# Performance work log

Hardware: AMD Instinct MI355X
Metric: run time of the kernel (lower is better)

The kernel has to match this reference:

```python
import jax, jax.numpy as jnp
import numpy as np

DIM = 384
NUM_HEADS = 12
HEAD_DIM = DIM // NUM_HEADS  # 32
SCALE = HEAD_DIM ** -0.5
B, N = 4, 2048


def setup_inputs() -> dict:
    key = jax.random.key(0)
    k0, k1, k2, k3 = jax.random.split(key, 4)
    x = jax.random.normal(k0, (B, N, DIM), dtype=jnp.float32)
    # nn.Linear(dim, 3*dim, bias=False): y = x @ W_qkv, W_qkv is [C, 3C]
    W_qkv = jax.random.normal(k1, (DIM, 3 * DIM), dtype=jnp.float32) * (DIM ** -0.5)
    # nn.Linear(dim, dim): y = x @ W_proj + b_proj, W_proj is [C, C]
    W_proj = jax.random.normal(k2, (DIM, DIM), dtype=jnp.float32) * (DIM ** -0.5)
    b_proj = jax.random.normal(k3, (DIM,), dtype=jnp.float32) * 0.01
    return {"x": x, "W_qkv": W_qkv, "W_proj": W_proj, "b_proj": b_proj}


def reference(x, W_qkv, W_proj, b_proj):
    b, n, c = x.shape
    qkv = (x @ W_qkv).reshape(b, n, 3, NUM_HEADS, HEAD_DIM)
    qkv = jnp.transpose(qkv, (2, 0, 3, 1, 4))  # [3, B, H, N, hd]
    q, k, v = qkv[0], qkv[1], qkv[2]
    # full attention: softmax(q k^T * scale) v
    attn = jnp.einsum('bhqd,bhkd->bhqk', q, k) * SCALE  # [B,H,N,N]
    attn = jax.nn.softmax(attn, axis=-1)
    out = jnp.einsum('bhqk,bhkd->bhqd', attn, v)  # [B,H,N,hd]
    out = jnp.transpose(out, (0, 2, 1, 3)).reshape(b, n, c)
    return out @ W_proj + b_proj
```

## Files before the change

kernel.cpp:

```cpp
#include <hip/hip_runtime.h>

constexpr int BB  = 4;
constexpr int SEQ = 2048;
constexpr int CC  = 384;
constexpr int C3  = 1152;
constexpr int NH  = 12;
constexpr int HD  = 32;
constexpr float SCALE = 0.17677669529663689f;
constexpr float LOG2E = 1.4426950408889634f;
constexpr float KSC   = SCALE * LOG2E;
constexpr size_t KV_BYTES = (size_t)2 * BB * NH * SEQ * HD * 2;
constexpr size_t WT_BYTES = ((size_t)C3 * CC + (size_t)CC * CC) * 2;
constexpr size_t XB_BYTES = (size_t)BB * SEQ * CC * 2;

typedef __attribute__((ext_vector_type(8))) short short8_t;
typedef __attribute__((ext_vector_type(4))) float floatx4;

#if __has_builtin(__builtin_amdgcn_exp2f)
#define EXP2F __builtin_amdgcn_exp2f
#else
#define EXP2F __builtin_exp2f
#endif

__device__ __forceinline__ unsigned short f2bf(float f) {
    unsigned int u = __builtin_bit_cast(unsigned int, f);
    u += 0x7fffu + ((u >> 16) & 1u);
    return (unsigned short)(u >> 16);
}
__device__ __forceinline__ unsigned int pk_rn(float lo, float hi) {
    return __builtin_amdgcn_perm(__builtin_bit_cast(unsigned int, hi) + 0x8000u,
                                 __builtin_bit_cast(unsigned int, lo) + 0x8000u,
                                 0x07060302u);
}
__device__ __forceinline__ unsigned int cvtpk(float lo, float hi) {
    unsigned int r;
    asm("v_cvt_pk_bf16_f32 %0, %1, %2" : "=v"(r) : "v"(lo), "v"(hi));
    return r;
}
__device__ __forceinline__ short8_t pack8(float4 a, float4 b) {
    uint4 u;
    u.x = pk_rn(a.x, a.y); u.y = pk_rn(a.z, a.w);
    u.z = pk_rn(b.x, b.y); u.w = pk_rn(b.z, b.w);
    return __builtin_bit_cast(short8_t, u);
}

__device__ __forceinline__ void vstore(unsigned short* vb, short8_t a, short8_t b) {
    const uint4 ua = __builtin_bit_cast(uint4, a);
    const uint4 ub = __builtin_bit_cast(uint4, b);
    *(uint2*)(vb)      = (uint2){ua.x, ua.y};
    *(uint2*)(vb + 8)  = (uint2){ua.z, ua.w};
    *(uint2*)(vb + 16) = (uint2){ub.x, ub.y};
    *(uint2*)(vb + 24) = (uint2){ub.z, ub.w};
}

__global__ __launch_bounds__(256) void prep_kernel(
    const float* __restrict__ x, const float* __restrict__ wqkv,
    const float* __restrict__ wproj,
    unsigned short* __restrict__ wqkvT, unsigned short* __restrict__ wprojT,
    unsigned short* __restrict__ xb)
{
    const int bid = blockIdx.x;
    if (bid >= 144) {
        const size_t base = (size_t)(bid - 144) * 2048 + threadIdx.x * 8;
        const float4 a = *(const float4*)(x + base);
        const float4 b = *(const float4*)(x + base + 4);
        uint4 u;
        u.x = pk_rn(a.x, a.y); u.y = pk_rn(a.z, a.w);
        u.z = pk_rn(b.x, b.y); u.w = pk_rn(b.z, b.w);
        *(uint4*)(xb + base) = u;
        return;
    }
    __shared__ float ls[64][68];
    const float* src; unsigned short* dst; int SN, k0, n0;
    if (bid < 108) {
        src = wqkv; dst = wqkvT; SN = C3;
        k0 = (bid / 18) * 64; n0 = (bid % 18) * 64;
    } else {
        const int b2 = bid - 108;
        src = wproj; dst = wprojT; SN = CC;
        k0 = (b2 / 6) * 64; n0 = (b2 % 6) * 64;
    }
    const int t  = threadIdx.x;
    const int rr = t >> 4, cc4 = (t & 15) * 4;
#pragma unroll
    for (int p = 0; p < 4; ++p) {
        const int row = p * 16 + rr;
        const float4 v = *(const float4*)&src[(size_t)(k0 + row) * SN + n0 + cc4];
        ls[row][cc4] = v.x; ls[row][cc4 + 1] = v.y;
        ls[row][cc4 + 2] = v.z; ls[row][cc4 + 3] = v.w;
    }
    __syncthreads();
#pragma unroll
    for (int p = 0; p < 4; ++p) {
        const int nrow = p * 16 + rr;
        uint2 u;
        u.x = pk_rn(ls[cc4][nrow],     ls[cc4 + 1][nrow]);
        u.y = pk_rn(ls[cc4 + 2][nrow], ls[cc4 + 3][nrow]);
        *(uint2*)&dst[(size_t)(n0 + nrow) * CC + k0 + cc4] = u;
    }
}

__global__ __launch_bounds__(256) void qkv_fast(
    const unsigned short* __restrict__ xb,
    const unsigned short* __restrict__ wT,
    unsigned short* __restrict__ qb,
    unsigned short* __restrict__ kv)
{
    __shared__ __align__(16) unsigned short As[2][128][40];
    __shared__ __align__(16) unsigned short Bs[2][128][40];

    const int mt   = blockIdx.x & 63;
    const int nb   = blockIdx.x >> 6;
    const int tid  = threadIdx.x;
    const int wid  = tid >> 6;
    const int lane = tid & 63;
    const int quad = lane >> 4;
    const int col  = lane & 15;
    const int wr   = wid >> 1, wc = wid & 1;
    const int m0 = mt * 128, n0 = nb * 128;

    const int arow = tid >> 1;
    const int aoff = (tid & 1) * 16;

    floatx4 acc[4][4];
#pragma unroll
    for (int i = 0; i < 4; ++i)
#pragma unroll
        for (int j = 0; j < 4; ++j) acc[i][j] = (floatx4){0.f, 0.f, 0.f, 0.f};

    const unsigned short* xrow = xb + (size_t)(m0 + arow) * CC + aoff;
    const unsigned short* wrow = wT + (size_t)(n0 + arow) * CC + aoff;

    short8_t ast0, ast1, bst0, bst1;
    ast0 = *(const short8_t*)xrow;
    ast1 = *(const short8_t*)(xrow + 8);
    bst0 = *(const short8_t*)wrow;
    bst1 = *(const short8_t*)(wrow + 8);
    *(short8_t*)&As[0][arow][aoff]     = ast0;
    *(short8_t*)&As[0][arow][aoff + 8] = ast1;
    *(short8_t*)&Bs[0][arow][aoff]     = bst0;
    *(short8_t*)&Bs[0][arow][aoff + 8] = bst1;

    for (int it = 0; it < CC / 32; ++it) {
        const int kn = (it + 1 < CC / 32) ? (it + 1) * 32 : 0;
        ast0 = *(const short8_t*)(xrow + kn);
        ast1 = *(const short8_t*)(xrow + kn + 8);
        bst0 = *(const short8_t*)(wrow + kn);
        bst1 = *(const short8_t*)(wrow + kn + 8);

        __syncthreads();
        const int p = it & 1;
        short8_t af[4], bf[4];
#pragma unroll
        for (int i = 0; i < 4; ++i)
            af[i] = *(const short8_t*)&As[p][wr * 64 + i * 16 + col][quad * 8];
#pragma unroll
        for (int j = 0; j < 4; ++j)
            bf[j] = *(const short8_t*)&Bs[p][wc * 64 + j * 16 + col][quad * 8];
#pragma unroll
        for (int j = 0; j < 4; ++j)
#pragma unroll
            for (int i = 0; i < 4; ++i)
                acc[i][j] = __builtin_amdgcn_mfma_f32_16x16x32_bf16(af[i], bf[j], acc[i][j], 0, 0, 0);

        *(short8_t*)&As[p ^ 1][arow][aoff]     = ast0;
        *(short8_t*)&As[p ^ 1][arow][aoff + 8] = ast1;
        *(short8_t*)&Bs[p ^ 1][arow][aoff]     = bst0;
        *(short8_t*)&Bs[p ^ 1][arow][aoff + 8] = bst1;
    }

    const int t = nb / 3;
#pragma unroll
    for (int i = 0; i < 4; ++i) {
        const int mg = m0 + wr * 64 + i * 16 + quad * 4;
        if (t == 0) {
#pragma unroll
            for (int j = 0; j < 4; ++j) {
                const int n = n0 + wc * 64 + j * 16 + col;
#pragma unroll
                for (int r = 0; r < 4; ++r)
                    qb[(size_t)(mg + r) * CC + n] = f2bf(acc[i][j][r]);
            }
        } else if (t == 1) {
            const int b = mg >> 11, s = mg & (SEQ - 1);
#pragma unroll
            for (int j = 0; j < 4; ++j) {
                const int rem = n0 - CC + wc * 64 + j * 16 + col;
                const int h = rem >> 5, d = rem & 31;
                unsigned short* kp = kv + ((size_t)(b * NH + h) * SEQ + s) * HD + d;
#pragma unroll
                for (int r = 0; r < 4; ++r)
                    kp[(size_t)r * HD] = f2bf(acc[i][j][r] * KSC);
            }
        } else {
            const int b = mg >> 11, s = mg & (SEQ - 1);
            unsigned short* vtb = kv + (size_t)BB * NH * SEQ * HD;
#pragma unroll
            for (int j = 0; j < 4; ++j) {
                const int rem = n0 - 2 * CC + wc * 64 + j * 16 + col;
                const int h = rem >> 5, d = rem & 31;
                uint2 u;
                u.x = pk_rn(acc[i][j][0], acc[i][j][1]);
                u.y = pk_rn(acc[i][j][2], acc[i][j][3]);
                *(uint2*)&vtb[((size_t)(b * NH + h) * HD + d) * SEQ + s] = u;
            }
        }
    }
}

__global__ __launch_bounds__(256, 4) void attn_kernel(
    const unsigned short* __restrict__ kv,
    const unsigned short* __restrict__ qb,
    unsigned short* __restrict__ ab)
{
    const int bid  = blockIdx.x;
    const int qp   = bid / 48;
    const int bh   = bid % 48;
    const int h    = bh % NH;
    const int b    = bh / NH;
    const int w    = threadIdx.x >> 6;
    const int lane = threadIdx.x & 63;
    const int quad = lane >> 4;
    const int col  = lane & 15;
    const int tid  = threadIdx.x;

    const unsigned short* K  = kv + (size_t)bh * SEQ * HD;
    const unsigned short* VT = kv + (size_t)BB * NH * SEQ * HD + (size_t)bh * HD * SEQ;

    __shared__ __align__(16) unsigned short Vt[2][32][136];

    const int drow_s = tid >> 3, voff_s = (tid & 7) * 16;
    const int vbase  = ((tid & 6) >> 1) * 32 + (tid & 1) * 4;

    const unsigned short* Kf = K + (size_t)col * HD + quad * 8;

    const int qrow = b * SEQ + qp * 64 + w * 16 + col;
    const short8_t qf = *(const short8_t*)(qb + (size_t)qrow * CC + h * HD + quad * 8);

    short8_t ones;
#pragma unroll
    for (int e = 0; e < 8; ++e) ones[e] = (short)0x3F80;

    floatx4 o[2];
    floatx4 lacc = (floatx4){0.f, 0.f, 0.f, 0.f};
    o[0] = (floatx4){0.f, 0.f, 0.f, 0.f};
    o[1] = (floatx4){0.f, 0.f, 0.f, 0.f};
    const float ci = -10.f * LOG2E;
    const floatx4 cinit = {ci, ci, ci, ci};

    short8_t v0a = *(const short8_t*)(VT + (size_t)drow_s * SEQ + voff_s);
    short8_t v0b = *(const short8_t*)(VT + (size_t)drow_s * SEQ + voff_s + 8);
    vstore(&Vt[0][drow_s][vbase], v0a, v0b);

    short8_t kaf[4][2];
#pragma unroll
    for (int c = 0; c < 4; ++c) {
        kaf[c][0] = *(const short8_t*)(Kf + (size_t)(c * 32) * HD);
        kaf[c][1] = *(const short8_t*)(Kf + (size_t)(c * 32 + 16) * HD);
    }

    for (int it = 0; it < SEQ / 128; ++it) {
        const int kn = ((it + 1) * 128) & (SEQ - 1);
        v0a = *(const short8_t*)(VT + (size_t)drow_s * SEQ + kn + voff_s);
        v0b = *(const short8_t*)(VT + (size_t)drow_s * SEQ + kn + voff_s + 8);
        const unsigned short* Kn = Kf + (size_t)kn * HD;

        __syncthreads();
        const int p = it & 1;

        short8_t va[4][2];
#pragma unroll
        for (int c = 0; c < 4; ++c) {
            const int c32 = c * 32;
            va[c][0] = *(const short8_t*)&Vt[p][col][c32 + quad * 8];
            va[c][1] = *(const short8_t*)&Vt[p][16 + col][c32 + quad * 8];
        }

#pragma unroll
        for (int c = 0; c < 4; ++c) {
            __builtin_amdgcn_s_setprio(1);
            const floatx4 s0 = __builtin_amdgcn_mfma_f32_16x16x32_bf16(kaf[c][0], qf, cinit, 0, 0, 0);
            const floatx4 s1 = __builtin_amdgcn_mfma_f32_16x16x32_bf16(kaf[c][1], qf, cinit, 0, 0, 0);
            __builtin_amdgcn_s_setprio(0);
            kaf[c][0] = *(const short8_t*)(Kn + (size_t)(c * 32) * HD);
            kaf[c][1] = *(const short8_t*)(Kn + (size_t)(c * 32 + 16) * HD);

            const float p00 = EXP2F(s0[0]), p01 = EXP2F(s0[1]);
            const float p02 = EXP2F(s0[2]), p03 = EXP2F(s0[3]);
            const float p10 = EXP2F(s1[0]), p11 = EXP2F(s1[1]);
            const float p12 = EXP2F(s1[2]), p13 = EXP2F(s1[3]);
            const uint4 pu = {cvtpk(p00, p01), cvtpk(p02, p03),
                              cvtpk(p10, p11), cvtpk(p12, p13)};
            const short8_t pb = __builtin_bit_cast(short8_t, pu);
            __builtin_amdgcn_s_setprio(1);
            o[0] = __builtin_amdgcn_mfma_f32_16x16x32_bf16(va[c][0], pb, o[0], 0, 0, 0);
            o[1] = __builtin_amdgcn_mfma_f32_16x16x32_bf16(va[c][1], pb, o[1], 0, 0, 0);
            lacc = __builtin_amdgcn_mfma_f32_16x16x32_bf16(ones, pb, lacc, 0, 0, 0);
            __builtin_amdgcn_s_setprio(0);
        }

        vstore(&Vt[p ^ 1][drow_s][vbase], v0a, v0b);
    }

    const float inv = 1.f / lacc[0];
    unsigned short* op = ab + (size_t)qrow * CC + h * HD;
#pragma unroll
    for (int i = 0; i < 2; ++i) {
        uint2 u;
        u.x = pk_rn(o[i][0] * inv, o[i][1] * inv);
        u.y = pk_rn(o[i][2] * inv, o[i][3] * inv);
        *(uint2*)&op[i * 16 + quad * 4] = u;
    }
}

__global__ __launch_bounds__(512) void proj_fast(
    const unsigned short* __restrict__ ab,
    const unsigned short* __restrict__ wT,
    const float* __restrict__ bias,
    float* __restrict__ out)
{
    __shared__ __align__(16) unsigned short Bs[2][384][32];

    const int mt   = blockIdx.x;
    const int tid  = threadIdx.x;
    const int wid  = tid >> 6;
    const int wn   = wid & 3;
    const int wm   = wid >> 2;
    const int lane = tid & 63;
    const int quad = lane >> 4;
    const int col  = lane & 15;
    const int m0   = mt * 32;

    floatx4 acc[6];
#pragma unroll
    for (int j = 0; j < 6; ++j) acc[j] = (floatx4){0.f, 0.f, 0.f, 0.f};

    const unsigned short* arow = ab + (size_t)(m0 + wm * 16 + col) * CC + quad * 8;

    const int f1 = tid;
    const int f2 = 512 + tid;
    const bool has2 = tid < 256;
    const unsigned short* wp1 = wT + (size_t)(f1 >> 1) * CC + (f1 & 1) * 16;
    const unsigned short* wp2 = wT + (size_t)(f2 >> 1) * CC + (f2 & 1) * 16;

    short8_t bA0, bA1, bB0, bB1;
    short8_t af;
    {
        bA0 = *(const short8_t*)wp1;
        bA1 = *(const short8_t*)(wp1 + 8);
        if (has2) {
            bB0 = *(const short8_t*)wp2;
            bB1 = *(const short8_t*)(wp2 + 8);
        }
        af = *(const short8_t*)arow;
        *(short8_t*)&Bs[0][f1 >> 1][(f1 & 1) * 16]     = bA0;
        *(short8_t*)&Bs[0][f1 >> 1][(f1 & 1) * 16 + 8] = bA1;
        if (has2) {
            *(short8_t*)&Bs[0][f2 >> 1][(f2 & 1) * 16]     = bB0;
            *(short8_t*)&Bs[0][f2 >> 1][(f2 & 1) * 16 + 8] = bB1;
        }
    }

    for (int it = 0; it < CC / 32; ++it) {
        const int kn = (it + 1 < CC / 32) ? (it + 1) * 32 : 0;
        bA0 = *(const short8_t*)(wp1 + kn);
        bA1 = *(const short8_t*)(wp1 + kn + 8);
        if (has2) {
            bB0 = *(const short8_t*)(wp2 + kn);
            bB1 = *(const short8_t*)(wp2 + kn + 8);
        }
        const short8_t afn = *(const short8_t*)(arow + kn);

        __syncthreads();
        const int p = it & 1;
        short8_t bf[6];
#pragma unroll
        for (int j = 0; j < 6; ++j)
            bf[j] = *(const short8_t*)&Bs[p][wn * 96 + j * 16 + col][quad * 8];
#pragma unroll
        for (int j = 0; j < 6; ++j)
            acc[j] = __builtin_amdgcn_mfma_f32_16x16x32_bf16(af, bf[j], acc[j], 0, 0, 0);

        *(short8_t*)&Bs[p ^ 1][f1 >> 1][(f1 & 1) * 16]     = bA0;
        *(short8_t*)&Bs[p ^ 1][f1 >> 1][(f1 & 1) * 16 + 8] = bA1;
        if (has2) {
            *(short8_t*)&Bs[p ^ 1][f2 >> 1][(f2 & 1) * 16]     = bB0;
            *(short8_t*)&Bs[p ^ 1][f2 >> 1][(f2 & 1) * 16 + 8] = bB1;
        }
        af = afn;
    }

#pragma unroll
    for (int j = 0; j < 6; ++j) {
        const int n = wn * 96 + j * 16 + col;
        const float bv = bias[n];
#pragma unroll
        for (int r = 0; r < 4; ++r)
            out[(size_t)(m0 + wm * 16 + quad * 4 + r) * CC + n] = acc[j][r] + bv;
    }
}

__global__ __launch_bounds__(256) void qkv_lds(
    const float* __restrict__ x, const float* __restrict__ w,
    float* __restrict__ dq, unsigned short* __restrict__ kv)
{
    __shared__ __align__(16) unsigned short wt[128 * 40];
    const int mt = blockIdx.x & 63, nb = blockIdx.x >> 6;
    const int tid = threadIdx.x, wid = tid >> 6, lane = tid & 63;
    const int quad = lane >> 4, col = lane & 15;
    const int wr = wid >> 1, wc = wid & 1;
    const int m0 = mt * 128, n0 = nb * 128;
    const int sn = tid >> 1, skg = (tid & 1) * 4;

    floatx4 acc[4][4];
#pragma unroll
    for (int i = 0; i < 4; ++i)
#pragma unroll
        for (int j = 0; j < 4; ++j) acc[i][j] = (floatx4){0.f, 0.f, 0.f, 0.f};
    const float* xbase = x + (size_t)(m0 + wr * 64 + col) * CC;

    for (int kb = 0; kb < CC; kb += 32) {
        float wv[4][4];
#pragma unroll
        for (int s = 0; s < 4; ++s) {
            const int k = kb + (skg + s) * 4;
#pragma unroll
            for (int j = 0; j < 4; ++j) wv[s][j] = w[(size_t)(k + j) * C3 + n0 + sn];
        }
        short8_t af[4];
#pragma unroll
        for (int i = 0; i < 4; ++i) {
            const float* xr = xbase + (size_t)i * 16 * CC + kb + quad * 8;
            af[i] = pack8(*(const float4*)xr, *(const float4*)(xr + 4));
        }
        __syncthreads();
#pragma unroll
        for (int s = 0; s < 4; ++s) {
            ushort4 u;
            u.x = f2bf(wv[s][0]); u.y = f2bf(wv[s][1]);
            u.z = f2bf(wv[s][2]); u.w = f2bf(wv[s][3]);
            *(ushort4*)&wt[sn * 40 + (skg + s) * 4] = u;
        }
        __syncthreads();
#pragma unroll
        for (int j = 0; j < 4; ++j) {
            const short8_t bf = *(const short8_t*)&wt[(wc * 64 + j * 16 + col) * 40 + quad * 8];
#pragma unroll
            for (int i = 0; i < 4; ++i)
                acc[i][j] = __builtin_amdgcn_mfma_f32_16x16x32_bf16(af[i], bf, acc[i][j], 0, 0, 0);
        }
    }
    const int t = nb / 3;
#pragma unroll
    for (int i = 0; i < 4; ++i) {
        const int mg = m0 + wr * 64 + i * 16 + quad * 4;
        if (t == 0) {
#pragma unroll
            for (int j = 0; j < 4; ++j) {
                const int n = n0 + wc * 64 + j * 16 + col;
#pragma unroll
                for (int r = 0; r < 4; ++r) dq[(size_t)(mg + r) * CC + n] = acc[i][j][r];
            }
        } else if (t == 1) {
            const int b = mg >> 11, s = mg & (SEQ - 1);
#pragma unroll
            for (int j = 0; j < 4; ++j) {
                const int rem = n0 - CC + wc * 64 + j * 16 + col;
                const int h = rem >> 5, d = rem & 31;
                unsigned short* kp = kv + ((size_t)(b * NH + h) * SEQ + s) * HD + d;
#pragma unroll
                for (int r = 0; r < 4; ++r) kp[(size_t)r * HD] = f2bf(acc[i][j][r]);
            }
        } else {
            const int b = mg >> 11, s = mg & (SEQ - 1);
            unsigned short* vtb = kv + (size_t)BB * NH * SEQ * HD;
#pragma unroll
            for (int j = 0; j < 4; ++j) {
                const int rem = n0 - 2 * CC + wc * 64 + j * 16 + col;
                const int h = rem >> 5, d = rem & 31;
                uint2 u;
                u.x = pk_rn(acc[i][j][0], acc[i][j][1]);
                u.y = pk_rn(acc[i][j][2], acc[i][j][3]);
                *(uint2*)&vtb[((size_t)(b * NH + h) * HD + d) * SEQ + s] = u;
            }
        }
    }
}

__global__ __launch_bounds__(256) void attn_f32(
    const unsigned short* __restrict__ kv,
    float* qatt)
{
    const int bid  = blockIdx.x;
    const int qp   = bid / 48;
    const int bh   = bid % 48;
    const int h    = bh % NH;
    const int b    = bh / NH;
    const int w    = threadIdx.x >> 6;
    const int lane = threadIdx.x & 63;
    const int quad = lane >> 4;
    const int col  = lane & 15;
    const int tid  = threadIdx.x;

    const unsigned short* K  = kv + (size_t)bh * SEQ * HD;
    const unsigned short* VT = kv + (size_t)BB * NH * SEQ * HD + (size_t)bh * HD * SEQ;

    __shared__ __align__(16) unsigned short Kt[2][128][40];
    __shared__ __align__(16) unsigned short Vt[2][32][136];

    const int krow_s = tid >> 1, koff_s = (tid & 1) * 16;
    const int drow_s = tid >> 3, voff_s = (tid & 7) * 16;

    int qrow[2];
    short8_t qf[2];
    const float sc = SCALE * LOG2E;
#pragma unroll
    for (int t = 0; t < 2; ++t) {
        qrow[t] = b * SEQ + qp * 128 + (w + 4 * t) * 16 + col;
        const float* qpt = qatt + (size_t)qrow[t] * CC + h * HD + quad * 8;
        const float4 a0 = *(const float4*)qpt;
        const float4 a1 = *(const float4*)(qpt + 4);
        const float4 s0 = {a0.x * sc, a0.y * sc, a0.z * sc, a0.w * sc};
        const float4 s1 = {a1.x * sc, a1.y * sc, a1.z * sc, a1.w * sc};
        qf[t] = pack8(s0, s1);
    }

    short8_t ones;
#pragma unroll
    for (int e = 0; e < 8; ++e) ones[e] = (short)0x3F80;

    floatx4 o[2][2];
    floatx4 lacc[2];
#pragma unroll
    for (int t = 0; t < 2; ++t) {
        lacc[t] = (floatx4){0.f, 0.f, 0.f, 0.f};
#pragma unroll
        for (int i = 0; i < 2; ++i) o[t][i] = (floatx4){0.f, 0.f, 0.f, 0.f};
    }
    const float ci = -10.f * LOG2E;
    const floatx4 cinit = {ci, ci, ci, ci};

    short8_t k0a = *(const short8_t*)(K + (size_t)krow_s * HD + koff_s);
    short8_t k0b = *(const short8_t*)(K + (size_t)krow_s * HD + koff_s + 8);
    short8_t v0a = *(const short8_t*)(VT + (size_t)drow_s * SEQ + voff_s);
    short8_t v0b = *(const short8_t*)(VT + (size_t)drow_s * SEQ + voff_s + 8);
    *(short8_t*)&Kt[0][krow_s][koff_s]     = k0a;
    *(short8_t*)&Kt[0][krow_s][koff_s + 8] = k0b;
    *(short8_t*)&Vt[0][drow_s][voff_s]     = v0a;
    *(short8_t*)&Vt[0][drow_s][voff_s + 8] = v0b;

    for (int it = 0; it < SEQ / 128; ++it) {
        const int kn = ((it + 1) * 128) & (SEQ - 1);
        k0a = *(const short8_t*)(K + (size_t)(kn + krow_s) * HD + koff_s);
        k0b = *(const short8_t*)(K + (size_t)(kn + krow_s) * HD + koff_s + 8);
        v0a = *(const short8_t*)(VT + (size_t)drow_s * SEQ + kn + voff_s);
        v0b = *(const short8_t*)(VT + (size_t)drow_s * SEQ + kn + voff_s + 8);

        __syncthreads();
        const int p = it & 1;

#pragma unroll
        for (int c = 0; c < 4; ++c) {
            const int c32 = c * 32;
            const short8_t ka0 = *(const short8_t*)&Kt[p][c32 + col][quad * 8];
            const short8_t ka1 = *(const short8_t*)&Kt[p][c32 + 16 + col][quad * 8];
            const uint2 w0a = *(const uint2*)&Vt[p][col][c32 + quad * 4];
            const uint2 w0b = *(const uint2*)&Vt[p][col][c32 + 16 + quad * 4];
            const uint2 w1a = *(const uint2*)&Vt[p][16 + col][c32 + quad * 4];
            const uint2 w1b = *(const uint2*)&Vt[p][16 + col][c32 + 16 + quad * 4];
            const short8_t va0 = __builtin_bit_cast(short8_t, (uint4){w0a.x, w0a.y, w0b.x, w0b.y});
            const short8_t va1 = __builtin_bit_cast(short8_t, (uint4){w1a.x, w1a.y, w1b.x, w1b.y});
#pragma unroll
            for (int t = 0; t < 2; ++t) {
                const floatx4 s0 = __builtin_amdgcn_mfma_f32_16x16x32_bf16(ka0, qf[t], cinit, 0, 0, 0);
                const floatx4 s1 = __builtin_amdgcn_mfma_f32_16x16x32_bf16(ka1, qf[t], cinit, 0, 0, 0);
                const float p00 = EXP2F(s0[0]), p01 = EXP2F(s0[1]);
                const float p02 = EXP2F(s0[2]), p03 = EXP2F(s0[3]);
                const float p10 = EXP2F(s1[0]), p11 = EXP2F(s1[1]);
                const float p12 = EXP2F(s1[2]), p13 = EXP2F(s1[3]);
                const uint4 pu = {pk_rn(p00, p01), pk_rn(p02, p03),
                                  pk_rn(p10, p11), pk_rn(p12, p13)};
                const short8_t pb = __builtin_bit_cast(short8_t, pu);
                o[t][0] = __builtin_amdgcn_mfma_f32_16x16x32_bf16(va0, pb, o[t][0], 0, 0, 0);
                o[t][1] = __builtin_amdgcn_mfma_f32_16x16x32_bf16(va1, pb, o[t][1], 0, 0, 0);
                lacc[t] = __builtin_amdgcn_mfma_f32_16x16x32_bf16(ones, pb, lacc[t], 0, 0, 0);
            }
        }

        *(short8_t*)&Kt[p ^ 1][krow_s][koff_s]     = k0a;
        *(short8_t*)&Kt[p ^ 1][krow_s][koff_s + 8] = k0b;
        *(short8_t*)&Vt[p ^ 1][drow_s][voff_s]     = v0a;
        *(short8_t*)&Vt[p ^ 1][drow_s][voff_s + 8] = v0b;
    }

#pragma unroll
    for (int t = 0; t < 2; ++t) {
        const float inv = 1.f / lacc[t][0];
        float* op = qatt + (size_t)qrow[t] * CC + h * HD;
#pragma unroll
        for (int r = 0; r < 4; ++r) {
            op[quad * 4 + r]      = o[t][0][r] * inv;
            op[16 + quad * 4 + r] = o[t][1][r] * inv;
        }
    }
}

__global__ __launch_bounds__(256) void proj_lds(
    float* att, const float* __restrict__ wp, const float* __restrict__ bias)
{
    __shared__ __align__(16) unsigned short wt[CC * 40];
    const int mt = blockIdx.x, tid = threadIdx.x, wid = tid >> 6, lane = tid & 63;
    const int quad = lane >> 4, col = lane & 15;
    const int m0 = mt * 16;
    floatx4 acc[6];
#pragma unroll
    for (int j = 0; j < 6; ++j) acc[j] = (floatx4){0.f, 0.f, 0.f, 0.f};
    for (int kb = 0; kb < CC; kb += 32) {
        float gv[12][4];
#pragma unroll
        for (int g = 0; g < 12; ++g) {
            const int flat = tid + g * 256, n = flat % 384, kg = flat / 384;
#pragma unroll
            for (int j = 0; j < 4; ++j) gv[g][j] = wp[(size_t)(kb + kg * 4 + j) * CC + n];
        }
        __syncthreads();
#pragma unroll
        for (int g = 0; g < 12; ++g) {
            const int flat = tid + g * 256, n = flat % 384, kg = flat / 384;
            ushort4 u;
            u.x = f2bf(gv[g][0]); u.y = f2bf(gv[g][1]);
            u.z = f2bf(gv[g][2]); u.w = f2bf(gv[g][3]);
            *(ushort4*)&wt[n * 40 + kg * 4] = u;
        }
        __syncthreads();
        const float* ap = att + (size_t)(m0 + col) * CC + kb + quad * 8;
        const short8_t af = pack8(*(const float4*)ap, *(const float4*)(ap + 4));
#pragma unroll
        for (int j = 0; j < 6; ++j) {
            const short8_t pb = *(const short8_t*)&wt[(wid * 96 + j * 16 + col) * 40 + quad * 8];
            acc[j] = __builtin_amdgcn_mfma_f32_16x16x32_bf16(af, pb, acc[j], 0, 0, 0);
        }
    }
    __syncthreads();
#pragma unroll
    for (int j = 0; j < 6; ++j) {
        const int n = wid * 96 + j * 16 + col;
        const float bv = bias[n];
#pragma unroll
        for (int r = 0; r < 4; ++r)
            att[(size_t)(m0 + quad * 4 + r) * CC + n] = acc[j][r] + bv;
    }
}

__global__ void marker_kernel(float* out, float val, int nelem) {
    int i = blockIdx.x * 256 + threadIdx.x;
    if (i < nelem) out[i] = val;
}

extern "C" void kernel_launch(void* const* d_in, const int* in_sizes, int n_in,
                              void* d_out, int out_size, void* d_ws, size_t ws_size,
                              hipStream_t stream)
{
    const float* x     = (const float*)d_in[0];
    const float* wqkv  = (const float*)d_in[1];
    const float* wproj = (const float*)d_in[2];
    const float* bproj = (const float*)d_in[3];
    float* out = (float*)d_out;
    unsigned short* kv = (unsigned short*)d_ws;

    if (ws_size < KV_BYTES) {
        const float marker = 100.f + (float)(ws_size >> 20);
        marker_kernel<<<(out_size + 255) / 256, 256, 0, stream>>>(out, marker, out_size);
        return;
    }

    unsigned short* wqkvT  = kv + (size_t)2 * BB * NH * SEQ * HD;
    unsigned short* wprojT = wqkvT + (size_t)C3 * CC;
    unsigned short* xb     = wprojT + (size_t)CC * CC;

    if (ws_size >= KV_BYTES + WT_BYTES + XB_BYTES) {
        unsigned short* qb = (unsigned short*)d_out;
        prep_kernel<<<144 + 1536, 256, 0, stream>>>(x, wqkv, wproj, wqkvT, wprojT, xb);
        qkv_fast<<<576, 256, 0, stream>>>(xb, wqkvT, qb, kv);
        attn_kernel<<<32 * BB * NH, 256, 0, stream>>>(kv, qb, xb );
        proj_fast<<<BB * SEQ / 32, 512, 0, stream>>>(xb, wprojT, bproj, out);
    } else {
        qkv_lds<<<576, 256, 0, stream>>>(x, wqkv, out, kv);
        attn_f32<<<16 * BB * NH, 256, 0, stream>>>(kv, out);
        proj_lds<<<BB * SEQ / 16, 256, 0, stream>>>(out, wproj, bproj);
    }
}
```

Before: 152.3 us.

## Pre-permute V layout in QKV epilogue and load V fragments directly from global

New measurement: 170.4 us. 11.9% more time.

```diff
diff --git a/kernel.cpp b/kernel.cpp
--- a/kernel.cpp
+++ b/kernel.cpp
@@ -44,15 +44,6 @@
     return __builtin_bit_cast(short8_t, u);
 }
 
-__device__ __forceinline__ void vstore(unsigned short* vb, short8_t a, short8_t b) {
-    const uint4 ua = __builtin_bit_cast(uint4, a);
-    const uint4 ub = __builtin_bit_cast(uint4, b);
-    *(uint2*)(vb)      = (uint2){ua.x, ua.y};
-    *(uint2*)(vb + 8)  = (uint2){ua.z, ua.w};
-    *(uint2*)(vb + 16) = (uint2){ub.x, ub.y};
-    *(uint2*)(vb + 24) = (uint2){ub.z, ub.w};
-}
-
 __global__ __launch_bounds__(256) void prep_kernel(
     const float* __restrict__ x, const float* __restrict__ wqkv,
     const float* __restrict__ wproj,
@@ -194,6 +185,9 @@
             }
         } else {
             const int b = mg >> 11, s = mg & (SEQ - 1);
+            const int sc = s & 31;
+            const int pos = ((sc & 15) >> 2) * 8 + ((sc >= 16) ? 4 : 0);
+            const int sperm = (s & ~31) + pos;
             unsigned short* vtb = kv + (size_t)BB * NH * SEQ * HD;
 #pragma unroll
             for (int j = 0; j < 4; ++j) {
@@ -202,13 +196,13 @@
                 uint2 u;
                 u.x = pk_rn(acc[i][j][0], acc[i][j][1]);
                 u.y = pk_rn(acc[i][j][2], acc[i][j][3]);
-                *(uint2*)&vtb[((size_t)(b * NH + h) * HD + d) * SEQ + s] = u;
-            }
-        }
-    }
-}
-
-__global__ __launch_bounds__(256, 4) void attn_kernel(
+                *(uint2*)&vtb[((size_t)(b * NH + h) * HD + d) * SEQ + sperm] = u;
+            }
+        }
+    }
+}
+
+__global__ __launch_bounds__(256, 3) void attn_kernel(
     const unsigned short* __restrict__ kv,
     const unsigned short* __restrict__ qb,
     unsigned short* __restrict__ ab)
@@ -222,94 +216,98 @@
     const int lane = threadIdx.x & 63;
     const int quad = lane >> 4;
     const int col  = lane & 15;
-    const int tid  = threadIdx.x;
 
     const unsigned short* K  = kv + (size_t)bh * SEQ * HD;
     const unsigned short* VT = kv + (size_t)BB * NH * SEQ * HD + (size_t)bh * HD * SEQ;
 
-    __shared__ __align__(16) unsigned short Vt[2][32][136];
-
-    const int drow_s = tid >> 3, voff_s = (tid & 7) * 16;
-    const int vbase  = ((tid & 6) >> 1) * 32 + (tid & 1) * 4;
-
-    const unsigned short* Kf = K + (size_t)col * HD + quad * 8;
-
-    const int qrow = b * SEQ + qp * 64 + w * 16 + col;
-    const short8_t qf = *(const short8_t*)(qb + (size_t)qrow * CC + h * HD + quad * 8);
+    const unsigned short* Kf  = K + (size_t)col * HD + quad * 8;
+    const unsigned short* Vf0 = VT + (size_t)col * SEQ + quad * 8;
+    const unsigned short* Vf1 = VT + (size_t)(16 + col) * SEQ + quad * 8;
+
+    int qrow[2];
+    short8_t qf[2];
+#pragma unroll
+    for (int t = 0; t < 2; ++t) {
+        qrow[t] = b * SEQ + qp * 128 + (w + 4 * t) * 16 + col;
+        qf[t] = *(const short8_t*)(qb + (size_t)qrow[t] * CC + h * HD + quad * 8);
+    }
 
     short8_t ones;
 #pragma unroll
     for (int e = 0; e < 8; ++e) ones[e] = (short)0x3F80;
 
-    floatx4 o[2];
-    floatx4 lacc = (floatx4){0.f, 0.f, 0.f, 0.f};
-    o[0] = (floatx4){0.f, 0.f, 0.f, 0.f};
-    o[1] = (floatx4){0.f, 0.f, 0.f, 0.f};
+    floatx4 o[2][2];
+    floatx4 lacc[2];
+#pragma unroll
+    for (int t = 0; t < 2; ++t) {
+        lacc[t] = (floatx4){0.f, 0.f, 0.f, 0.f};
+#pragma unroll
+        for (int i = 0; i < 2; ++i) o[t][i] = (floatx4){0.f, 0.f, 0.f, 0.f};
+    }
     const float ci = -10.f * LOG2E;
     const floatx4 cinit = {ci, ci, ci, ci};
 
-    short8_t v0a = *(const short8_t*)(VT + (size_t)drow_s * SEQ + voff_s);
-    short8_t v0b = *(const short8_t*)(VT + (size_t)drow_s * SEQ + voff_s + 8);
-    vstore(&Vt[0][drow_s][vbase], v0a, v0b);
-
-    short8_t kaf[4][2];
+    short8_t kaf[4][2], vaf[4][2];
 #pragma unroll
     for (int c = 0; c < 4; ++c) {
         kaf[c][0] = *(const short8_t*)(Kf + (size_t)(c * 32) * HD);
         kaf[c][1] = *(const short8_t*)(Kf + (size_t)(c * 32 + 16) * HD);
+        vaf[c][0] = *(const short8_t*)(Vf0 + c * 32);
+        vaf[c][1] = *(const short8_t*)(Vf1 + c * 32);
     }
 
     for (int it = 0; it < SEQ / 128; ++it) {
         const int kn = ((it + 1) * 128) & (SEQ - 1);
-        v0a = *(const short8_t*)(VT + (size_t)drow_s * SEQ + kn + voff_s);
-        v0b = *(const short8_t*)(VT + (size_t)drow_s * SEQ + kn + voff_s + 8);
         const unsigned short* Kn = Kf + (size_t)kn * HD;
 
-        __syncthreads();
-        const int p = it & 1;
-
-        short8_t va[4][2];
 #pragma unroll
         for (int c = 0; c < 4; ++c) {
-            const int c32 = c * 32;
-            va[c][0] = *(const short8_t*)&Vt[p][col][c32 + quad * 8];
-            va[c][1] = *(const short8_t*)&Vt[p][16 + col][c32 + quad * 8];
-        }
-
-#pragma unroll
-        for (int c = 0; c < 4; ++c) {
+            floatx4 s0[2], s1[2];
             __builtin_amdgcn_s_setprio(1);
-            const floatx4 s0 = __builtin_amdgcn_mfma_f32_16x16x32_bf16(kaf[c][0], qf, cinit, 0, 0, 0);
-            const floatx4 s1 = __builtin_amdgcn_mfma_f32_16x16x32_bf16(kaf[c][1], qf, cinit, 0, 0, 0);
+#pragma unroll
+            for (int t = 0; t < 2; ++t) {
+                s0[t] = __builtin_amdgcn_mfma_f32_16x16x32_bf16(kaf[c][0], qf[t], cinit, 0, 0, 0);
+                s1[t] = __builtin_amdgcn_mfma_f32_16x16x32_bf16(kaf[c][1], qf[t], cinit, 0, 0, 0);
+            }
             __builtin_amdgcn_s_setprio(0);
             kaf[c][0] = *(const short8_t*)(Kn + (size_t)(c * 32) * HD);
             kaf[c][1] = *(const short8_t*)(Kn + (size_t)(c * 32 + 16) * HD);
 
-            const float p00 = EXP2F(s0[0]), p01 = EXP2F(s0[1]);
-            const float p02 = EXP2F(s0[2]), p03 = EXP2F(s0[3]);
-            const float p10 = EXP2F(s1[0]), p11 = EXP2F(s1[1]);
-            const float p12 = EXP2F(s1[2]), p13 = EXP2F(s1[3]);
-            const uint4 pu = {cvtpk(p00, p01), cvtpk(p02, p03),
-                              cvtpk(p10, p11), cvtpk(p12, p13)};
-            const short8_t pb = __builtin_bit_cast(short8_t, pu);
+            short8_t pb[2];
+#pragma unroll
+            for (int t = 0; t < 2; ++t) {
+                const float p00 = EXP2F(s0[t][0]), p01 = EXP2F(s0[t][1]);
+                const float p02 = EXP2F(s0[t][2]), p03 = EXP2F(s0[t][3]);
+                const float p10 = EXP2F(s1[t][0]), p11 = EXP2F(s1[t][1]);
+                const float p12 = EXP2F(s1[t][2]), p13 = EXP2F(s1[t][3]);
+                const uint4 pu = {cvtpk(p00, p01), cvtpk(p02, p03),
+                                  cvtpk(p10, p11), cvtpk(p12, p13)};
+                pb[t] = __builtin_bit_cast(short8_t, pu);
+            }
             __builtin_amdgcn_s_setprio(1);
-            o[0] = __builtin_amdgcn_mfma_f32_16x16x32_bf16(va[c][0], pb, o[0], 0, 0, 0);
-            o[1] = __builtin_amdgcn_mfma_f32_16x16x32_bf16(va[c][1], pb, o[1], 0, 0, 0);
-            lacc = __builtin_amdgcn_mfma_f32_16x16x32_bf16(ones, pb, lacc, 0, 0, 0);
+#pragma unroll
+            for (int t = 0; t < 2; ++t) {
+                o[t][0] = __builtin_amdgcn_mfma_f32_16x16x32_bf16(vaf[c][0], pb[t], o[t][0], 0, 0, 0);
+                o[t][1] = __builtin_amdgcn_mfma_f32_16x16x32_bf16(vaf[c][1], pb[t], o[t][1], 0, 0, 0);
+                lacc[t] = __builtin_amdgcn_mfma_f32_16x16x32_bf16(ones, pb[t], lacc[t], 0, 0, 0);
+            }
             __builtin_amdgcn_s_setprio(0);
-        }
-
-        vstore(&Vt[p ^ 1][drow_s][vbase], v0a, v0b);
-    }
-
-    const float inv = 1.f / lacc[0];
-    unsigned short* op = ab + (size_t)qrow * CC + h * HD;
-#pragma unroll
-    for (int i = 0; i < 2; ++i) {
-        uint2 u;
-        u.x = pk_rn(o[i][0] * inv, o[i][1] * inv);
-        u.y = pk_rn(o[i][2] * inv, o[i][3] * inv);
-        *(uint2*)&op[i * 16 + quad * 4] = u;
+            vaf[c][0] = *(const short8_t*)(Vf0 + kn + c * 32);
+            vaf[c][1] = *(const short8_t*)(Vf1 + kn + c * 32);
+        }
+    }
+
+#pragma unroll
+    for (int t = 0; t < 2; ++t) {
+        const float inv = 1.f / lacc[t][0];
+        unsigned short* op = ab + (size_t)qrow[t] * CC + h * HD;
+#pragma unroll
+        for (int i = 0; i < 2; ++i) {
+            uint2 u;
+            u.x = pk_rn(o[t][i][0] * inv, o[t][i][1] * inv);
+            u.y = pk_rn(o[t][i][2] * inv, o[t][i][3] * inv);
+            *(uint2*)&op[i * 16 + quad * 4] = u;
+        }
     }
 }
 
@@ -682,7 +680,7 @@
         unsigned short* qb = (unsigned short*)d_out;
         prep_kernel<<<144 + 1536, 256, 0, stream>>>(x, wqkv, wproj, wqkvT, wprojT, xb);
         qkv_fast<<<576, 256, 0, stream>>>(xb, wqkvT, qb, kv);
-        attn_kernel<<<32 * BB * NH, 256, 0, stream>>>(kv, qb, xb );
+        attn_kernel<<<16 * BB * NH, 256, 0, stream>>>(kv, qb, xb );
         proj_fast<<<BB * SEQ / 32, 512, 0, stream>>>(xb, wprojT, bproj, out);
     } else {
         qkv_lds<<<576, 256, 0, stream>>>(x, wqkv, out, kv);
```
